# Optimization experiments

Measured on AMD Instinct MI355X. Metric: run time of the kernel, lower is better.

## Reference

```python
import jax, jax.numpy as jnp
import numpy as np

EMBED = 1024
HEAD = 64
NHEADS = EMBED // HEAD  # 16
EPS = 1e-5


def layernorm(x, g, b):
    m = jnp.mean(x, axis=-1, keepdims=True)
    v = jnp.var(x, axis=-1, keepdims=True)
    return (x - m) * jax.lax.rsqrt(v + EPS) * g + b


def msa(x, Wq, Wk, Wv):
    # x: [B,T,C]; Wq/Wk/Wv: [H, C, hd] (per-head, no bias)
    B, T, C = x.shape
    q = jnp.einsum('btc,hcd->bhtd', x, Wq)
    k = jnp.einsum('btc,hcd->bhtd', x, Wk)
    v = jnp.einsum('btc,hcd->bhtd', x, Wv)
    # NOTE: source scales by embed_size C ** -0.5, not head_size
    wei = jnp.einsum('bhtd,bhsd->bhts', q, k) * (C ** -0.5)
    wei = jax.nn.softmax(wei, axis=-1)
    out = jnp.einsum('bhts,bhsd->bhtd', wei, v)
    # concat heads (head order matches torch ModuleList cat)
    return out.transpose(0, 2, 1, 3).reshape(B, T, C)


def setup_inputs() -> dict:
    key = jax.random.key(0)
    ks = jax.random.split(key, 12)
    B, T, C = 4, 1024, EMBED
    s = C ** -0.5
    inp = {
        'x': jax.random.normal(ks[0], (B, T, C), jnp.float32),
        'Wq1': jax.random.normal(ks[1], (NHEADS, C, HEAD), jnp.float32) * s,
        'Wk1': jax.random.normal(ks[2], (NHEADS, C, HEAD), jnp.float32) * s,
        'Wv1': jax.random.normal(ks[3], (NHEADS, C, HEAD), jnp.float32) * s,
        'Wq2': jax.random.normal(ks[4], (NHEADS, C, HEAD), jnp.float32) * s,
        'Wk2': jax.random.normal(ks[5], (NHEADS, C, HEAD), jnp.float32) * s,
        'Wv2': jax.random.normal(ks[6], (NHEADS, C, HEAD), jnp.float32) * s,
        'g1': jnp.ones((C,), jnp.float32), 'b1': jnp.zeros((C,), jnp.float32),
        'g2': jnp.ones((C,), jnp.float32), 'b2': jnp.zeros((C,), jnp.float32),
        'g3': jnp.ones((C,), jnp.float32), 'b3': jnp.zeros((C,), jnp.float32),
        'W1': jax.random.normal(ks[7], (C, 4 * C), jnp.float32) * s,
        'bf1': jnp.zeros((4 * C,), jnp.float32),
        'W2': jax.random.normal(ks[8], (4 * C, C), jnp.float32) * (4 * C) ** -0.5,
        'bf2': jnp.zeros((C,), jnp.float32),
    }
    return inp


def reference(x, Wq1, Wk1, Wv1, Wq2, Wk2, Wv2, g1, b1, g2, b2, g3, b3, W1, bf1, W2, bf2):
    x = x + msa(layernorm(x, g1, b1), Wq1, Wk1, Wv1)
    x = x + msa(layernorm(x, g2, b2), Wq2, Wk2, Wv2)
    h = layernorm(x, g3, b3)
    h = jax.nn.relu(h @ W1 + bf1) @ W2 + bf2
    return x + h
```

## Files before the change

### kernel.cpp

```cpp
#include <hip/hip_runtime.h>


#define DEVI __device__ __forceinline__

typedef unsigned short u16;
typedef short bf16x8 __attribute__((ext_vector_type(8)));
typedef float f32x4 __attribute__((ext_vector_type(4)));
typedef unsigned short u16x4 __attribute__((ext_vector_type(4)));

DEVI u16 f2bf(float f) {
  union { float f; unsigned u; } v; v.f = f;
  unsigned r = v.u + 0x7FFFu + ((v.u >> 16) & 1u);
  return (u16)(r >> 16);
}
DEVI float bf2f(u16 u) {
  union { unsigned u; float f; } v; v.u = ((unsigned)u) << 16; return v.f;
}

DEVI void gload16(const void* g, void* l) {
  __builtin_amdgcn_global_load_lds((const __attribute__((address_space(1))) void*)g,
                                   (__attribute__((address_space(3))) void*)l,
                                   16, 0, 0);
}


__global__ __launch_bounds__(256) void k_pack_headw(const float* __restrict__ W,
                                                    u16* __restrict__ out) {
  const int k0 = blockIdx.x * 64;
  const int h  = blockIdx.y;
  __shared__ float t[64][65];
  const int tid = threadIdx.x;
#pragma unroll
  for (int p = 0; p < 16; p++) {
    int e = p * 256 + tid, kk = e >> 6, d = e & 63;
    t[kk][d] = W[h * 65536 + (k0 + kk) * 64 + d];
  }
  __syncthreads();
#pragma unroll
  for (int p = 0; p < 16; p++) {
    int e = p * 256 + tid, d = e >> 6, kk = e & 63;
    out[(size_t)(h * 64 + d) * 1024 + k0 + kk] = f2bf(t[kk][d]);
  }
}

__global__ __launch_bounds__(256) void k_transpose(const float* __restrict__ in,
                                                   u16* __restrict__ out,
                                                   int R, int C) {
  const int c0 = blockIdx.x * 64, r0 = blockIdx.y * 64;
  __shared__ float t[64][65];
  const int tid = threadIdx.x;
#pragma unroll
  for (int p = 0; p < 16; p++) {
    int e = p * 256 + tid, rr = e >> 6, cc = e & 63;
    t[rr][cc] = in[(size_t)(r0 + rr) * C + c0 + cc];
  }
  __syncthreads();
#pragma unroll
  for (int p = 0; p < 16; p++) {
    int e = p * 256 + tid, cc = e >> 6, rr = e & 63;
    out[(size_t)(c0 + cc) * R + r0 + rr] = f2bf(t[rr][cc]);
  }
}

__global__ __launch_bounds__(256) void k_ln(const float* __restrict__ xin,
                                            const u16* __restrict__ oin,
                                            float* __restrict__ xsum,
                                            u16* __restrict__ xn,
                                            const float* __restrict__ g,
                                            const float* __restrict__ b) {
  const int row = blockIdx.x;
  const size_t base = (size_t)row * 1024;
  const int tid = threadIdx.x;
  float4 xv = ((const float4*)(xin + base))[tid];
  if (oin) {
    u16x4 ov = *(const u16x4*)(oin + base + tid * 4);
    xv.x += bf2f(ov[0]); xv.y += bf2f(ov[1]);
    xv.z += bf2f(ov[2]); xv.w += bf2f(ov[3]);
  }
  if (xsum) ((float4*)(xsum + base))[tid] = xv;
  float s = xv.x + xv.y + xv.z + xv.w;
  float q = xv.x * xv.x + xv.y * xv.y + xv.z * xv.z + xv.w * xv.w;
#pragma unroll
  for (int m = 1; m < 64; m <<= 1) { s += __shfl_xor(s, m); q += __shfl_xor(q, m); }
  __shared__ float red[8];
  const int wave = tid >> 6, lane = tid & 63;
  if (lane == 0) { red[wave] = s; red[4 + wave] = q; }
  __syncthreads();
  s = red[0] + red[1] + red[2] + red[3];
  q = red[4] + red[5] + red[6] + red[7];
  const float mean = s * (1.f / 1024.f);
  const float var  = q * (1.f / 1024.f) - mean * mean;
  const float rstd = rsqrtf(var + 1e-5f);
  float4 gv = ((const float4*)g)[tid];
  float4 bv = ((const float4*)b)[tid];
  u16x4 o;
  o[0] = f2bf((xv.x - mean) * rstd * gv.x + bv.x);
  o[1] = f2bf((xv.y - mean) * rstd * gv.y + bv.y);
  o[2] = f2bf((xv.z - mean) * rstd * gv.z + bv.z);
  o[3] = f2bf((xv.w - mean) * rstd * gv.w + bv.w);
  *(u16x4*)(xn + base + tid * 4) = o;
}

template <int EPI>
__global__ __launch_bounds__(256, 4) void gemm_bt(const u16* __restrict__ A,
                                                  const u16* __restrict__ Bt,
                                                  void* __restrict__ outp,
                                                  void* __restrict__ outp2,
                                                  const float* __restrict__ bias,
                                                  int M, int N, int K) {
  __shared__ u16 As[2][128 * 32];
  __shared__ u16 Bs[2][128 * 32];
  const int tid = threadIdx.x;
  const int wave = tid >> 6, lane = tid & 63;
  const int lg = lane >> 4, l15 = lane & 15;
  const int wr = wave >> 1, wc = wave & 1;

  const int nwg = gridDim.x * gridDim.y;
  int bid = blockIdx.y * gridDim.x + blockIdx.x;
  bid = (bid & 7) * (nwg >> 3) + (bid >> 3);
  const int by = bid / gridDim.x, bx = bid % gridDim.x;

  const int Ksz   = (EPI == 3) ? (K >> 1) : K;
  const int kbase = (EPI == 3) ? (int)blockIdx.z * Ksz : 0;

  const u16* Ab = A + (size_t)by * 128 * K;
  const u16* Bb = Bt + (size_t)bx * 128 * K;

  const int r0 = tid >> 2, q = tid & 3, r1 = r0 + 64;
  const int c0s = (q ^ ((r0 >> 1) & 3)) * 8;
  const int c1s = (q ^ ((r1 >> 1) & 3)) * 8;
  char* const a0[2] = {(char*)As[0] + wave * 1024, (char*)As[1] + wave * 1024};
  char* const a1[2] = {(char*)As[0] + 4096 + wave * 1024, (char*)As[1] + 4096 + wave * 1024};
  char* const b0[2] = {(char*)Bs[0] + wave * 1024, (char*)Bs[1] + wave * 1024};
  char* const b1[2] = {(char*)Bs[0] + 4096 + wave * 1024, (char*)Bs[1] + 4096 + wave * 1024};

#define STAGE(b, kk)                                       \
  gload16(Ab + (size_t)r0 * K + (kk) + c0s, a0[b]);        \
  gload16(Ab + (size_t)r1 * K + (kk) + c1s, a1[b]);        \
  gload16(Bb + (size_t)r0 * K + (kk) + c0s, b0[b]);        \
  gload16(Bb + (size_t)r1 * K + (kk) + c1s, b1[b]);

  int aoff[4], boff[4];
#pragma unroll
  for (int i = 0; i < 4; i++) {
    int Ra = wr * 64 + i * 16 + l15;
    aoff[i] = Ra * 64 + ((lg ^ ((Ra >> 1) & 3)) << 4);
    int Rb = wc * 64 + i * 16 + l15;
    boff[i] = Rb * 64 + ((lg ^ ((Rb >> 1) & 3)) << 4);
  }

  const f32x4 zero = {0.f, 0.f, 0.f, 0.f};
  f32x4 acc[4][4];
#pragma unroll
  for (int i = 0; i < 4; i++)
#pragma unroll
    for (int j = 0; j < 4; j++) acc[i][j] = zero;

#define COMPUTE(b)                                                             \
  {                                                                            \
    bf16x8 af[4], bfv[4];                                                      \
    _Pragma("unroll") for (int i = 0; i < 4; i++)                              \
        af[i] = *(const bf16x8*)((const char*)As[b] + aoff[i]);                \
    _Pragma("unroll") for (int j = 0; j < 4; j++)                              \
        bfv[j] = *(const bf16x8*)((const char*)Bs[b] + boff[j]);               \
    _Pragma("unroll") for (int i = 0; i < 4; i++)                              \
        _Pragma("unroll") for (int j = 0; j < 4; j++)                          \
            acc[i][j] = __builtin_amdgcn_mfma_f32_16x16x32_bf16(               \
                af[i], bfv[j], acc[i][j], 0, 0, 0);                            \
  }

  const int NT = Ksz >> 5;
  STAGE(0, kbase);
  __syncthreads();
  for (int t = 0; t < NT; t += 2) {
    STAGE(1, kbase + (t + 1) * 32);
    COMPUTE(0);
    __syncthreads();
    if (t + 2 < NT) { STAGE(0, kbase + (t + 2) * 32); }
    COMPUTE(1);
    __syncthreads();
  }
#undef STAGE
#undef COMPUTE

  const int rbase = by * 128 + wr * 64 + lg * 4;
  const int cbase = bx * 128 + wc * 64 + l15;
  if constexpr (EPI == 0) {
    u16* out = (u16*)outp;
#pragma unroll
    for (int i = 0; i < 4; i++)
#pragma unroll
      for (int j = 0; j < 4; j++)
#pragma unroll
        for (int r = 0; r < 4; r++)
          out[(size_t)(rbase + i * 16 + r) * N + cbase + j * 16] = f2bf(acc[i][j][r]);
  } else if constexpr (EPI == 1) {
    u16* out = (u16*)outp;
#pragma unroll
    for (int j = 0; j < 4; j++) {
      const float bv = bias[cbase + j * 16];
#pragma unroll
      for (int i = 0; i < 4; i++)
#pragma unroll
        for (int r = 0; r < 4; r++)
          out[(size_t)(rbase + i * 16 + r) * N + cbase + j * 16] =
              f2bf(fmaxf(acc[i][j][r] + bv, 0.f));
    }
  } else {
    float* out = blockIdx.z ? (float*)outp2 : (float*)outp;
#pragma unroll
    for (int i = 0; i < 4; i++)
#pragma unroll
      for (int j = 0; j < 4; j++)
#pragma unroll
        for (int r = 0; r < 4; r++)
          out[(size_t)(rbase + i * 16 + r) * N + cbase + j * 16] = acc[i][j][r];
  }
}

__global__ __launch_bounds__(256) void k_comb(const float* __restrict__ P0,
                                              const float* __restrict__ P1,
                                              const float* __restrict__ bias,
                                              float* __restrict__ xacc) {
  const size_t i = (size_t)blockIdx.x * 1024 + threadIdx.x * 4;
  float4 a = *(const float4*)(P0 + i);
  float4 b = *(const float4*)(P1 + i);
  float4 x = *(const float4*)(xacc + i);
  float4 bv = *(const float4*)(bias + threadIdx.x * 4);
  x.x += a.x + b.x + bv.x;
  x.y += a.y + b.y + bv.y;
  x.z += a.z + b.z + bv.z;
  x.w += a.w + b.w + bv.w;
  *(float4*)(xacc + i) = x;
}

__global__ __launch_bounds__(256) void k_packkv(const u16* __restrict__ QKV,
                                                u16* __restrict__ Kp,
                                                u16* __restrict__ Vp) {
  const int t  = blockIdx.x;
  const int bh = blockIdx.y, b = bh >> 4, h = bh & 15;
  const int tid = threadIdx.x;
  __shared__ u16 vt[64][80];

  const u16* Ksrc = QKV + (size_t)(b * 1024 + t * 64) * 3072 + 1024 + h * 64;
  const u16* Vsrc = QKV + (size_t)(b * 1024 + t * 64) * 3072 + 2048 + h * 64;
  u16* KpT = Kp + (size_t)(bh * 16 + t) * 4096;
  u16* VpT = Vp + (size_t)(bh * 16 + t) * 4096;

#pragma unroll
  for (int p = 0; p < 2; p++) {
    int e = p * 256 + tid, rr = e >> 3, dd = (e & 7) * 8;
    *(bf16x8*)&vt[rr][dd] = *(const bf16x8*)(Ksrc + (size_t)rr * 3072 + dd);
  }
  __syncthreads();
#pragma unroll
  for (int p = 0; p < 2; p++) {
    int c = p * 256 + tid;
    int i = c >> 6, lane = c & 63, lgg = lane >> 4, ll = lane & 15;
    int j = i >> 1;
    int row = 8 * (ll >> 2) + (ll & 3) + (j & 1) * 4 + (j >> 1) * 32;
    int col = (i & 1) * 32 + lgg * 8;
    *(bf16x8*)&KpT[(size_t)c * 8] = *(const bf16x8*)&vt[row][col];
  }
  __syncthreads();
#pragma unroll
  for (int p = 0; p < 2; p++) {
    int e = p * 256 + tid, rr = e >> 3, dd = (e & 7) * 8;
    *(bf16x8*)&vt[rr][dd] = *(const bf16x8*)(Vsrc + (size_t)rr * 3072 + dd);
  }
  __syncthreads();
#pragma unroll
  for (int p = 0; p < 2; p++) {
    int c = p * 256 + tid;
    int i = c >> 6, lane = c & 63, lgg = lane >> 4, ll = lane & 15;
    int dg = (i >> 1) & 3, kh = i & 1;
    bf16x8 o;
#pragma unroll
    for (int jj = 0; jj < 8; jj++)
      o[jj] = (short)vt[kh * 32 + lgg * 8 + jj][dg * 16 + ll];
    *(bf16x8*)&VpT[(size_t)c * 8] = o;
  }
}

DEVI void load8(bf16x8 (&r)[8], const u16* p) {
#pragma unroll
  for (int i = 0; i < 8; i++) r[i] = *(const bf16x8*)(p + i * 512);
}

DEVI void attn_tile32(const bf16x8 (&kr)[8], const bf16x8 (&vr)[8],
                      const bf16x8 (&qf)[2][2], f32x4 (&oa)[2][4],
                      float (&m)[2], float (&sden)[2], int lg, float cexp) {
  const f32x4 zero = {0.f, 0.f, 0.f, 0.f};
#pragma unroll
  for (int qh = 0; qh < 2; qh++) {
    f32x4 s0 = zero, s1 = zero, s2 = zero, s3 = zero;
    s0 = __builtin_amdgcn_mfma_f32_16x16x32_bf16(kr[0], qf[qh][0], s0, 0, 0, 0);
    s0 = __builtin_amdgcn_mfma_f32_16x16x32_bf16(kr[1], qf[qh][1], s0, 0, 0, 0);
    s1 = __builtin_amdgcn_mfma_f32_16x16x32_bf16(kr[2], qf[qh][0], s1, 0, 0, 0);
    s1 = __builtin_amdgcn_mfma_f32_16x16x32_bf16(kr[3], qf[qh][1], s1, 0, 0, 0);
    s2 = __builtin_amdgcn_mfma_f32_16x16x32_bf16(kr[4], qf[qh][0], s2, 0, 0, 0);
    s2 = __builtin_amdgcn_mfma_f32_16x16x32_bf16(kr[5], qf[qh][1], s2, 0, 0, 0);
    s3 = __builtin_amdgcn_mfma_f32_16x16x32_bf16(kr[6], qf[qh][0], s3, 0, 0, 0);
    s3 = __builtin_amdgcn_mfma_f32_16x16x32_bf16(kr[7], qf[qh][1], s3, 0, 0, 0);

    f32x4 mv = s0;
#pragma unroll
    for (int r = 0; r < 4; r++) mv[r] = fmaxf(fmaxf(mv[r], s1[r]), fmaxf(s2[r], s3[r]));
    float mx = fmaxf(fmaxf(mv[0], mv[1]), fmaxf(mv[2], mv[3]));
    mx = fmaxf(mx, __shfl_xor(mx, 16));
    mx = fmaxf(mx, __shfl_xor(mx, 32));
    const float mn = fmaxf(m[qh], mx);
    const float fr = exp2f((m[qh] - mn) * cexp);
    m[qh] = mn;
#pragma unroll
    for (int r = 0; r < 4; r++) {
      s0[r] = exp2f((s0[r] - mn) * cexp);
      s1[r] = exp2f((s1[r] - mn) * cexp);
      s2[r] = exp2f((s2[r] - mn) * cexp);
      s3[r] = exp2f((s3[r] - mn) * cexp);
    }
    f32x4 sv = (s0 + s1) + (s2 + s3);
    float ts = (sv[0] + sv[1]) + (sv[2] + sv[3]);
    ts += __shfl_xor(ts, 16);
    ts += __shfl_xor(ts, 32);
    sden[qh] = sden[qh] * fr + ts;

    bf16x8 pa0, pa1;
#pragma unroll
    for (int r = 0; r < 4; r++) {
      pa0[r]     = (short)f2bf(s0[r]);
      pa0[4 + r] = (short)f2bf(s1[r]);
      pa1[r]     = (short)f2bf(s2[r]);
      pa1[4 + r] = (short)f2bf(s3[r]);
    }

    float frq[4];
#pragma unroll
    for (int r = 0; r < 4; r++) frq[r] = __shfl(fr, 20 * lg + r, 64);
#pragma unroll
    for (int dg = 0; dg < 4; dg++) {
      oa[qh][dg][0] *= frq[0]; oa[qh][dg][1] *= frq[1];
      oa[qh][dg][2] *= frq[2]; oa[qh][dg][3] *= frq[3];
      oa[qh][dg] = __builtin_amdgcn_mfma_f32_16x16x32_bf16(pa0, vr[2 * dg],     oa[qh][dg], 0, 0, 0);
      oa[qh][dg] = __builtin_amdgcn_mfma_f32_16x16x32_bf16(pa1, vr[2 * dg + 1], oa[qh][dg], 0, 0, 0);
    }
  }
}

__global__ __launch_bounds__(256) void k_attn(const u16* __restrict__ QKV,
                                              const u16* __restrict__ Kp,
                                              const u16* __restrict__ Vp,
                                              u16* __restrict__ O) {
  const int Tn = 1024;
  const int bh = blockIdx.x, b = bh >> 4, h = bh & 15;
  const int q0 = blockIdx.y * 128;
  const int tid = threadIdx.x, wave = tid >> 6, lane = tid & 63;
  const int lg = lane >> 4, l15 = lane & 15;

  const u16* Qb = QKV + (size_t)(b * Tn + q0 + wave * 32 + l15) * 3072 + h * 64 + lg * 8;
  bf16x8 qf[2][2];
  qf[0][0] = *(const bf16x8*)Qb;
  qf[0][1] = *(const bf16x8*)(Qb + 32);
  qf[1][0] = *(const bf16x8*)(Qb + 16 * 3072);
  qf[1][1] = *(const bf16x8*)(Qb + 16 * 3072 + 32);

  const u16* KpB = Kp + (size_t)bh * 65536 + lane * 8;
  const u16* VpB = Vp + (size_t)bh * 65536 + lane * 8;

  const float cexp = 0.03125f * 1.44269504f;

  float m[2] = {-1e30f, -1e30f}, sden[2] = {0.f, 0.f};
  const f32x4 zero = {0.f, 0.f, 0.f, 0.f};
  f32x4 oa[2][4];
#pragma unroll
  for (int qh = 0; qh < 2; qh++)
#pragma unroll
    for (int dg = 0; dg < 4; dg++) oa[qh][dg] = zero;

  bf16x8 ka[8], va[8], kb[8], vb[8];
  load8(ka, KpB);
  load8(va, VpB);

  for (int t = 0; t < 16; t += 2) {
    load8(kb, KpB + (t + 1) * 4096);
    load8(vb, VpB + (t + 1) * 4096);
    attn_tile32(ka, va, qf, oa, m, sden, lg, cexp);
    if (t + 2 < 16) {
      load8(ka, KpB + (t + 2) * 4096);
      load8(va, VpB + (t + 2) * 4096);
    }
    attn_tile32(kb, vb, qf, oa, m, sden, lg, cexp);
  }

#pragma unroll
  for (int qh = 0; qh < 2; qh++) {
    float sdq[4];
#pragma unroll
    for (int r = 0; r < 4; r++) sdq[r] = 1.f / __shfl(sden[qh], 20 * lg + r, 64);
    u16* Ob = O + (size_t)(b * Tn + q0 + wave * 32 + qh * 16) * 1024 + h * 64;
#pragma unroll
    for (int dg = 0; dg < 4; dg++)
#pragma unroll
      for (int r = 0; r < 4; r++)
        Ob[(size_t)(lg * 4 + r) * 1024 + dg * 16 + l15] = f2bf(oa[qh][dg][r] * sdq[r]);
  }
}

extern "C" void kernel_launch(void* const* d_in, const int* in_sizes, int n_in,
                              void* d_out, int out_size, void* d_ws, size_t ws_size,
                              hipStream_t stream) {
  const float* x   = (const float*)d_in[0];
  const float* Wq1 = (const float*)d_in[1];
  const float* Wk1 = (const float*)d_in[2];
  const float* Wv1 = (const float*)d_in[3];
  const float* Wq2 = (const float*)d_in[4];
  const float* Wk2 = (const float*)d_in[5];
  const float* Wv2 = (const float*)d_in[6];
  const float* g1  = (const float*)d_in[7];
  const float* b1  = (const float*)d_in[8];
  const float* g2  = (const float*)d_in[9];
  const float* b2  = (const float*)d_in[10];
  const float* g3  = (const float*)d_in[11];
  const float* b3  = (const float*)d_in[12];
  const float* W1  = (const float*)d_in[13];
  const float* bf1 = (const float*)d_in[14];
  const float* W2  = (const float*)d_in[15];
  const float* bf2 = (const float*)d_in[16];

  char* ws = (char*)d_ws;
  u16* Wqkv1t = (u16*)(ws);
  u16* Wqkv2t = (u16*)(ws + 6291456);
  u16* W1t    = (u16*)(ws + 12582912);
  u16* W2t    = (u16*)(ws + 20971520);
  u16* xn     = (u16*)(ws + 29360128);
  u16* QKV    = (u16*)(ws + 37748736);
  u16* Kp     = (u16*)(ws + 62914560);
  u16* Vp     = (u16*)(ws + 71303168);
  u16* O      = (u16*)(ws + 79691776);
  u16* h1     = (u16*)(ws + 37748736);
  float* P0   = (float*)(ws);
  float* P1   = (float*)(ws + 71303168);
  float* xacc = (float*)d_out;

  const dim3 blk(256);

  k_pack_headw<<<dim3(16, 16), blk, 0, stream>>>(Wq1, Wqkv1t);
  k_pack_headw<<<dim3(16, 16), blk, 0, stream>>>(Wk1, Wqkv1t + 1024 * 1024);
  k_pack_headw<<<dim3(16, 16), blk, 0, stream>>>(Wv1, Wqkv1t + 2048 * 1024);
  k_pack_headw<<<dim3(16, 16), blk, 0, stream>>>(Wq2, Wqkv2t);
  k_pack_headw<<<dim3(16, 16), blk, 0, stream>>>(Wk2, Wqkv2t + 1024 * 1024);
  k_pack_headw<<<dim3(16, 16), blk, 0, stream>>>(Wv2, Wqkv2t + 2048 * 1024);
  k_transpose<<<dim3(64, 16), blk, 0, stream>>>(W1, W1t, 1024, 4096);
  k_transpose<<<dim3(16, 64), blk, 0, stream>>>(W2, W2t, 4096, 1024);

  k_ln<<<4096, blk, 0, stream>>>(x, nullptr, nullptr, xn, g1, b1);
  gemm_bt<0><<<dim3(24, 32), blk, 0, stream>>>(xn, Wqkv1t, QKV, nullptr, nullptr, 4096, 3072, 1024);
  k_packkv<<<dim3(16, 64), blk, 0, stream>>>(QKV, Kp, Vp);
  k_attn<<<dim3(64, 8), blk, 0, stream>>>(QKV, Kp, Vp, O);
  k_ln<<<4096, blk, 0, stream>>>(x, O, xacc, xn, g2, b2);

  gemm_bt<0><<<dim3(24, 32), blk, 0, stream>>>(xn, Wqkv2t, QKV, nullptr, nullptr, 4096, 3072, 1024);
  k_packkv<<<dim3(16, 64), blk, 0, stream>>>(QKV, Kp, Vp);
  k_attn<<<dim3(64, 8), blk, 0, stream>>>(QKV, Kp, Vp, O);
  k_ln<<<4096, blk, 0, stream>>>(xacc, O, xacc, xn, g3, b3);

  gemm_bt<1><<<dim3(32, 32), blk, 0, stream>>>(xn, W1t, h1, nullptr, bf1, 4096, 4096, 1024);
  gemm_bt<3><<<dim3(8, 32, 2), blk, 0, stream>>>(h1, W2t, P0, P1, nullptr, 4096, 1024, 4096);
  k_comb<<<4096, blk, 0, stream>>>(P0, P1, bf2, xacc);

  (void)in_sizes; (void)n_in; (void)out_size; (void)ws_size;
}
```

Baseline: 447.0 us.

## Add 256x256-tile 8-wave GEMM kernel for QKV and FFN1 projections

Introduces a new GEMM kernel with 256x256 output tiles, 512 threads, a K-step of 64, an XOR-swizzled LDS layout and double buffering. LDS reads, async global-to-LDS loads and MFMA blocks are interleaved with barriers, and MFMA priority is raised via setprio. It replaces the 128x128 kernel for the two QKV projections and the first FFN GEMM (with bias+ReLU epilogue), aiming for more data reuse per tile and better overlap of loads with compute. The cost is fewer workgroups (192-256 on a large CU count), which risks tail and occupancy imbalance, plus heavy register and LDS use.

```diff
diff --git a/kernel.cpp b/kernel.cpp
--- a/kernel.cpp
+++ b/kernel.cpp
@@ -101,6 +101,137 @@
   *(u16x4*)(xn + base + tid * 4) = o;
 }
 
+#define BAR() __builtin_amdgcn_s_barrier()
+#define VMW4() asm volatile("s_waitcnt vmcnt(4)" ::: "memory")
+
+template <int EPI>
+__global__ __launch_bounds__(512, 2) void gemm256(const u16* __restrict__ A,
+                                                  const u16* __restrict__ Bt,
+                                                  void* __restrict__ outp,
+                                                  const float* __restrict__ bias,
+                                                  int M, int N, int K) {
+  __shared__ u16 LS[65536];
+  const int tid = threadIdx.x;
+  const int wave = tid >> 6, lane = tid & 63;
+  const int lg = lane >> 4, l15 = lane & 15;
+  const int wm = wave >> 2, wn = wave & 3;
+
+  const int gx = gridDim.x, nwg = gx * gridDim.y;
+  int bid = blockIdx.y * gx + blockIdx.x;
+  bid = (bid & 7) * (nwg >> 3) + (bid >> 3);
+  const int by = bid / gx, bx = bid % gx;
+
+  const u16* Ab = A + (size_t)by * 256 * K;
+  const u16* Bb = Bt + (size_t)bx * 256 * K;
+
+  const int r0 = tid >> 2, r1 = r0 + 128, sq = tid & 3;
+  const int q0s = (sq ^ (r0 & 3)) * 8;
+  const int q1s = (sq ^ (r1 & 3)) * 8;
+  const int wbase = wave * 512;
+
+#define STG(buf, abo, ks, Xb, tk)                                              \
+  {                                                                            \
+    u16* dst = &LS[(buf) * 32768 + (abo) + (ks) * 8192 + wbase];               \
+    gload16((Xb) + (size_t)r0 * K + (tk) + (ks) * 32 + q0s, dst);              \
+    gload16((Xb) + (size_t)r1 * K + (tk) + (ks) * 32 + q1s, dst + 4096);       \
+  }
+
+  const int aswz = (lg ^ (l15 & 3)) << 3;
+  const int rowA = wm * 128 + l15;
+  const int rowB = wn * 64 + l15;
+
+  f32x4 acc[8][4];
+  const f32x4 zero = {0.f, 0.f, 0.f, 0.f};
+#pragma unroll
+  for (int i = 0; i < 8; i++)
+#pragma unroll
+    for (int j = 0; j < 4; j++) acc[i][j] = zero;
+
+  bf16x8 af[4], bf[4];
+
+#define RD_B(cur, ks)                                                          \
+  _Pragma("unroll") for (int j = 0; j < 4; j++)                                \
+      bf[j] = *(const bf16x8*)&LS[(cur) * 32768 + 16384 + (ks) * 8192 +        \
+                                  (rowB + j * 16) * 32 + aswz];
+#define RD_A(cur, ks, fh)                                                      \
+  _Pragma("unroll") for (int i = 0; i < 4; i++)                                \
+      af[i] = *(const bf16x8*)&LS[(cur) * 32768 + (ks) * 8192 +                \
+                                  (rowA + ((fh) * 4 + i) * 16) * 32 + aswz];
+#define MFMA16(fh)                                                             \
+  __builtin_amdgcn_s_setprio(1);                                               \
+  _Pragma("unroll") for (int i = 0; i < 4; i++)                                \
+      _Pragma("unroll") for (int j = 0; j < 4; j++)                            \
+          acc[(fh) * 4 + i][j] = __builtin_amdgcn_mfma_f32_16x16x32_bf16(      \
+              af[i], bf[j], acc[(fh) * 4 + i][j], 0, 0, 0);                    \
+  __builtin_amdgcn_s_setprio(0);
+
+  const int NT = K >> 6;
+
+  STG(0, 0,     0, Ab, 0);
+  STG(0, 16384, 0, Bb, 0);
+  STG(0, 0,     1, Ab, 0);
+  STG(0, 16384, 1, Bb, 0);
+  VMW4();
+  BAR();
+
+  for (int t = 0; t < NT; ++t) {
+    const int cur = t & 1, nxt = cur ^ 1;
+    const int tk = (t + 1) << 6;
+    const bool st = (t + 1 < NT);
+    RD_B(cur, 0); RD_A(cur, 0, 0);
+    if (st) STG(nxt, 0, 0, Ab, tk);
+    BAR();
+    MFMA16(0);
+    BAR();
+    RD_A(cur, 0, 1);
+    if (st) STG(nxt, 16384, 0, Bb, tk);
+    BAR();
+    MFMA16(1);
+    VMW4();
+    BAR();
+    RD_B(cur, 1); RD_A(cur, 1, 0);
+    if (st) STG(nxt, 0, 1, Ab, tk);
+    BAR();
+    MFMA16(0);
+    BAR();
+    RD_A(cur, 1, 1);
+    if (st) STG(nxt, 16384, 1, Bb, tk);
+    BAR();
+    MFMA16(1);
+    VMW4();
+    BAR();
+  }
+#undef STG
+#undef RD_A
+#undef RD_B
+#undef MFMA16
+
+  const int rb = by * 256 + wm * 128 + lg * 4;
+  const int cb = bx * 256 + wn * 64 + l15;
+  if constexpr (EPI == 0) {
+    u16* out = (u16*)outp;
+#pragma unroll
+    for (int i8 = 0; i8 < 8; i8++)
+#pragma unroll
+      for (int j = 0; j < 4; j++)
+#pragma unroll
+        for (int r = 0; r < 4; r++)
+          out[(size_t)(rb + i8 * 16 + r) * N + cb + j * 16] = f2bf(acc[i8][j][r]);
+  } else {
+    u16* out = (u16*)outp;
+#pragma unroll
+    for (int j = 0; j < 4; j++) {
+      const float bv = bias[cb + j * 16];
+#pragma unroll
+      for (int i8 = 0; i8 < 8; i8++)
+#pragma unroll
+        for (int r = 0; r < 4; r++)
+          out[(size_t)(rb + i8 * 16 + r) * N + cb + j * 16] =
+              f2bf(fmaxf(acc[i8][j][r] + bv, 0.f));
+    }
+  }
+}
+
 template <int EPI>
 __global__ __launch_bounds__(256, 4) void gemm_bt(const u16* __restrict__ A,
                                                   const u16* __restrict__ Bt,
@@ -185,7 +316,16 @@
 
   const int rbase = by * 128 + wr * 64 + lg * 4;
   const int cbase = bx * 128 + wc * 64 + l15;
-  if constexpr (EPI == 0) {
+  if constexpr (EPI == 3) {
+    float* out = blockIdx.z ? (float*)outp2 : (float*)outp;
+#pragma unroll
+    for (int i = 0; i < 4; i++)
+#pragma unroll
+      for (int j = 0; j < 4; j++)
+#pragma unroll
+        for (int r = 0; r < 4; r++)
+          out[(size_t)(rbase + i * 16 + r) * N + cbase + j * 16] = acc[i][j][r];
+  } else {
     u16* out = (u16*)outp;
 #pragma unroll
     for (int i = 0; i < 4; i++)
@@ -194,28 +334,8 @@
 #pragma unroll
         for (int r = 0; r < 4; r++)
           out[(size_t)(rbase + i * 16 + r) * N + cbase + j * 16] = f2bf(acc[i][j][r]);
-  } else if constexpr (EPI == 1) {
-    u16* out = (u16*)outp;
-#pragma unroll
-    for (int j = 0; j < 4; j++) {
-      const float bv = bias[cbase + j * 16];
-#pragma unroll
-      for (int i = 0; i < 4; i++)
-#pragma unroll
-        for (int r = 0; r < 4; r++)
-          out[(size_t)(rbase + i * 16 + r) * N + cbase + j * 16] =
-              f2bf(fmaxf(acc[i][j][r] + bv, 0.f));
-    }
-  } else {
-    float* out = blockIdx.z ? (float*)outp2 : (float*)outp;
-#pragma unroll
-    for (int i = 0; i < 4; i++)
-#pragma unroll
-      for (int j = 0; j < 4; j++)
-#pragma unroll
-        for (int r = 0; r < 4; r++)
-          out[(size_t)(rbase + i * 16 + r) * N + cbase + j * 16] = acc[i][j][r];
-  }
+  }
+  (void)bias;
 }
 
 __global__ __launch_bounds__(256) void k_comb(const float* __restrict__ P0,
@@ -443,6 +563,7 @@
   float* xacc = (float*)d_out;
 
   const dim3 blk(256);
+  const dim3 blk5(512);
 
   k_pack_headw<<<dim3(16, 16), blk, 0, stream>>>(Wq1, Wqkv1t);
   k_pack_headw<<<dim3(16, 16), blk, 0, stream>>>(Wk1, Wqkv1t + 1024 * 1024);
@@ -454,17 +575,17 @@
   k_transpose<<<dim3(16, 64), blk, 0, stream>>>(W2, W2t, 4096, 1024);
 
   k_ln<<<4096, blk, 0, stream>>>(x, nullptr, nullptr, xn, g1, b1);
-  gemm_bt<0><<<dim3(24, 32), blk, 0, stream>>>(xn, Wqkv1t, QKV, nullptr, nullptr, 4096, 3072, 1024);
+  gemm256<0><<<dim3(12, 16), blk5, 0, stream>>>(xn, Wqkv1t, QKV, nullptr, 4096, 3072, 1024);
   k_packkv<<<dim3(16, 64), blk, 0, stream>>>(QKV, Kp, Vp);
   k_attn<<<dim3(64, 8), blk, 0, stream>>>(QKV, Kp, Vp, O);
   k_ln<<<4096, blk, 0, stream>>>(x, O, xacc, xn, g2, b2);
 
-  gemm_bt<0><<<dim3(24, 32), blk, 0, stream>>>(xn, Wqkv2t, QKV, nullptr, nullptr, 4096, 3072, 1024);
+  gemm256<0><<<dim3(12, 16), blk5, 0, stream>>>(xn, Wqkv2t, QKV, nullptr, 4096, 3072, 1024);
   k_packkv<<<dim3(16, 64), blk, 0, stream>>>(QKV, Kp, Vp);
   k_attn<<<dim3(64, 8), blk, 0, stream>>>(QKV, Kp, Vp, O);
   k_ln<<<4096, blk, 0, stream>>>(xacc, O, xacc, xn, g3, b3);
 
-  gemm_bt<1><<<dim3(32, 32), blk, 0, stream>>>(xn, W1t, h1, nullptr, bf1, 4096, 4096, 1024);
+  gemm256<1><<<dim3(16, 16), blk5, 0, stream>>>(xn, W1t, h1, bf1, 4096, 4096, 1024);
   gemm_bt<3><<<dim3(8, 32, 2), blk, 0, stream>>>(h1, W2t, P0, P1, nullptr, 4096, 1024, 4096);
   k_comb<<<4096, blk, 0, stream>>>(P0, P1, bf2, xacc);
 
```

Result: no change. 453.3 us (+1.4%).
